# Performance work log

Hardware: AMD Instinct MI355X
Metric: run time of the kernel (lower is better)

The kernel has to match this reference:

```python
import jax, jax.numpy as jnp
import numpy as np

NUM_HEADS = 16
DIM_HIDDEN = 1024
DIM_ATTN = DIM_HIDDEN // NUM_HEADS  # 64
SCALE = DIM_ATTN ** (-0.5)
TOP_K = 32


def setup_inputs() -> dict:
    rng = jax.random.key(0)
    k1, k2, k3, k4, k5 = jax.random.split(rng, 5)
    b, sq, sk, d = 2, 2048, 2048, DIM_HIDDEN
    lim = 1.0 / np.sqrt(d)  # nn.Linear default init range
    return {
        "query": jax.random.normal(k1, (b, sq, d), jnp.float32),
        "key": jax.random.normal(k2, (b, sk, d), jnp.float32),
        "value": jax.random.normal(k3, (b, sk, d), jnp.float32),
        "Wq": jax.random.uniform(k4, (d, d), jnp.float32, -lim, lim),
        "Wk": jax.random.uniform(k5, (d, d), jnp.float32, -lim, lim),
    }


def _split_heads(x, b, s):
    # (b, s, D) -> (b, H, s, d_head)
    return x.reshape(b, s, NUM_HEADS, DIM_ATTN).transpose(0, 2, 1, 3)


def reference(query, key, value, Wq, Wk):
    b, sq, d = query.shape
    sk = key.shape[1]
    # nn.Linear: y = x @ W^T  (bias=False); V and out are Identity
    q = _split_heads(query @ Wq.T, b, sq)
    k = _split_heads(key @ Wk.T, b, sk)
    v = _split_heads(value, b, sk)
    # dense scores (b, H, sq, sk)
    scores = jnp.einsum('bhqa,bhka->bhqk', q, k) * SCALE
    # top-k sparsified softmax: keep entries >= k-th largest score per row
    top_vals = jax.lax.top_k(scores, TOP_K)[0]
    cutoff = top_vals[..., -1:]  # (b, H, sq, 1)
    masked = jnp.where(scores >= cutoff, scores, -jnp.inf)
    w = jax.nn.softmax(masked, axis=-1)
    e = jnp.einsum('bhqk,bhka->bhqa', w, v)
    return e.transpose(0, 2, 1, 3).reshape(b, sq, d)
```

## Files before the change

kernel.cpp:

```cpp
#include <hip/hip_runtime.h>
#include <cstdint>
#include <cstddef>

#define BB 2
#define HH 16
#define SS 2048
#define DD 1024
#define DA 64
#define TOPK 32
#define ROWS 4

__global__ __launch_bounds__(256, 4) void proj_kernel(const float* __restrict__ X0,
                                                      const float* __restrict__ W0,
                                                      float* __restrict__ O0,
                                                      const float* __restrict__ X1,
                                                      const float* __restrict__ W1,
                                                      float* __restrict__ O1) {
  const float* __restrict__ X = blockIdx.z ? X1 : X0;
  const float* __restrict__ W = blockIdx.z ? W1 : W0;
  float* __restrict__ O       = blockIdx.z ? O1 : O0;

  __shared__ float Ast[16][65];
  __shared__ float Bst[16][65];
  const int tid = threadIdx.x;
  const int tx = tid & 15, ty = tid >> 4;
  const int m0 = blockIdx.y * 64, n0 = blockIdx.x * 64;

  float res[4][4], acc[4][4];
#pragma unroll
  for (int i = 0; i < 4; ++i)
#pragma unroll
    for (int j = 0; j < 4; ++j) { res[i][j] = 0.f; acc[i][j] = 0.f; }

  const int srow = tid >> 2, skg = tid & 3;
  for (int k0 = 0; k0 < 1024; k0 += 16) {
    if (k0 == 384 || k0 == 768) {
#pragma unroll
      for (int i = 0; i < 4; ++i)
#pragma unroll
        for (int j = 0; j < 4; ++j) { res[i][j] = __fadd_rn(res[i][j], acc[i][j]); acc[i][j] = 0.f; }
    }
    {
      const float4 va = *(const float4*)(X + (size_t)(m0 + srow) * 1024 + k0 + skg * 4);
      Ast[skg * 4 + 0][srow] = va.x; Ast[skg * 4 + 1][srow] = va.y;
      Ast[skg * 4 + 2][srow] = va.z; Ast[skg * 4 + 3][srow] = va.w;
      const float4 vb = *(const float4*)(W + (size_t)(n0 + srow) * 1024 + k0 + skg * 4);
      Bst[skg * 4 + 0][srow] = vb.x; Bst[skg * 4 + 1][srow] = vb.y;
      Bst[skg * 4 + 2][srow] = vb.z; Bst[skg * 4 + 3][srow] = vb.w;
    }
    __syncthreads();
#pragma unroll
    for (int k = 0; k < 16; ++k) {
      float av[4], bv[4];
#pragma unroll
      for (int i = 0; i < 4; ++i) av[i] = Ast[k][ty * 4 + i];
#pragma unroll
      for (int j = 0; j < 4; ++j) bv[j] = Bst[k][tx * 4 + j];
#pragma unroll
      for (int i = 0; i < 4; ++i)
#pragma unroll
        for (int j = 0; j < 4; ++j) acc[i][j] = fmaf(av[i], bv[j], acc[i][j]);
    }
    __syncthreads();
  }

#pragma unroll
  for (int i = 0; i < 4; ++i) {
    const int m = m0 + ty * 4 + i;
    const int b = m >> 11, s = m & 2047;
#pragma unroll
    for (int j = 0; j < 4; ++j) {
      const int n = n0 + tx * 4 + j;
      const int h = n >> 6, da = n & 63;
      const float v = __fadd_rn(res[i][j], acc[i][j]);
      if (blockIdx.z) {
        O[(((size_t)((b * 16 + h) * 16 + (da >> 2)) * 2048 + s) << 2) + (da & 3)] = v;
      } else {
        O[(((size_t)(b * 16 + h) * 2048 + s) * 64 + da)] = v;
      }
    }
  }
}

__global__ __launch_bounds__(256) void attn_kernel(const float* __restrict__ Qp,
                                                   const float* __restrict__ Kp,
                                                   const float* __restrict__ V,
                                                   float* __restrict__ out) {
  __shared__ float Srow[ROWS * 2048];

  const int tid = threadIdx.x;
  const int w = tid >> 6, l = tid & 63;
  const int nwg = BB * HH * (SS / ROWS);
  const int bidx = (int)blockIdx.x;
  const int swz = (bidx & 7) * (nwg >> 3) + (bidx >> 3);
  const int bh = swz >> 9;
  const int rb = swz & 511;
  const int b = bh >> 4, h = bh & 15;
  const int r0 = rb * ROWS;

  const float* Ktb = Kp + (size_t)bh * (16 * 2048 * 4);

#pragma unroll 1
  for (int c = 0; c < 8; ++c) {
    const int key = tid + c * 256;

    float acc[ROWS][4];
#pragma unroll
    for (int r = 0; r < ROWS; ++r)
#pragma unroll
      for (int j = 0; j < 4; ++j) acc[r][j] = 0.f;

#pragma unroll
    for (int g = 0; g < 4; ++g) {
      float4 kt[4];
#pragma unroll
      for (int i = 0; i < 4; ++i)
        kt[i] = *(const float4*)(Ktb + (((size_t)(g * 4 + i) * 2048 + key) << 2));
#pragma unroll
      for (int r = 0; r < ROWS; ++r) {
        const float4* qp4 = (const float4*)(Qp + ((size_t)bh * SS + r0 + r) * DA);
        float4 q4[4];
#pragma unroll
        for (int i = 0; i < 4; ++i) q4[i] = qp4[g * 4 + i];
#pragma unroll
        for (int blk = 3; blk >= 0; --blk) {
          acc[r][0] = __fadd_rn(acc[r][0], __fmul_rn(q4[blk].x, kt[blk].x));
          acc[r][1] = __fadd_rn(acc[r][1], __fmul_rn(q4[blk].y, kt[blk].y));
          acc[r][2] = __fadd_rn(acc[r][2], __fmul_rn(q4[blk].z, kt[blk].z));
          acc[r][3] = __fadd_rn(acc[r][3], __fmul_rn(q4[blk].w, kt[blk].w));
        }
      }
    }
#pragma unroll
    for (int r = 0; r < ROWS; ++r) {
      const float s = __fadd_rn(__fadd_rn(acc[r][0], acc[r][1]),
                                __fadd_rn(acc[r][2], acc[r][3]));
      Srow[r * 2048 + key] = s * 0.125f;
    }
  }
  __syncthreads();

  const float* Vh = V + (size_t)b * SS * DD + h * DA;
  float* outh = out + ((size_t)(b * SS + r0 + w)) * DD + h * DA;

  {
    const int r = w;
    float sv[32];
#pragma unroll
    for (int i = 0; i < 32; ++i) sv[i] = Srow[r * 2048 + 64 * i + l];
    float* wl = &Srow[r * 2048];
    float* kl = &Srow[r * 2048 + 64];

    float mx = sv[0], mn = sv[0];
#pragma unroll
    for (int i = 1; i < 32; ++i) { mx = fmaxf(mx, sv[i]); mn = fminf(mn, sv[i]); }
#pragma unroll
    for (int off = 32; off >= 1; off >>= 1) {
      mx = fmaxf(mx, __shfl_xor(mx, off));
      mn = fminf(mn, __shfl_xor(mn, off));
    }

    float lo = mn, hi = mx + 1.0f;
    float cutoff = mn;
    for (int it = 0; ; ++it) {
      const float mid = 0.5f * (lo + hi);
      if (it >= 64 || !(mid > lo && mid < hi)) { cutoff = lo; break; }
      int c = 0;
#pragma unroll
      for (int i = 0; i < 32; ++i)
        c += (int)__popcll(__ballot(sv[i] >= mid));
      if (c == TOPK) {
        float cm = 3.0e38f;
#pragma unroll
        for (int i = 0; i < 32; ++i) if (sv[i] >= mid) cm = fminf(cm, sv[i]);
#pragma unroll
        for (int off = 32; off >= 1; off >>= 1) cm = fminf(cm, __shfl_xor(cm, off));
        cutoff = cm;
        break;
      }
      if (c > TOPK) lo = mid; else hi = mid;
    }

    float wv[32];
    float dpart = 0.f;
    int ckept = 0;
#pragma unroll
    for (int i = 0; i < 32; ++i) {
      const bool keep = (sv[i] >= cutoff);
      ckept += (int)__popcll(__ballot(keep));
      const float e = keep ? __expf(sv[i] - mx) : 0.f;
      wv[i] = e;
      dpart += e;
    }
    float denom = dpart;
#pragma unroll
    for (int off = 32; off >= 1; off >>= 1) denom += __shfl_xor(denom, off);
    const float inv_denom = 1.0f / denom;

    float e = 0.f;
    if (ckept <= 64) {
      int base = 0;
#pragma unroll
      for (int i = 0; i < 32; ++i) {
        const unsigned long long mball = __ballot(wv[i] > 0.f);
        if (wv[i] > 0.f) {
          const int pos = base + (int)__popcll(mball & ((1ull << l) - 1ull));
          wl[pos] = wv[i];
          kl[pos] = __int_as_float(64 * i + l);
        }
        base += (int)__popcll(mball);
      }
      asm volatile("s_waitcnt lgkmcnt(0)" ::: "memory");
      int i = 0;
      for (; i + 8 <= ckept; i += 8) {
        float ww[8]; int kk[8];
#pragma unroll
        for (int u = 0; u < 8; ++u) { ww[u] = wl[i + u]; kk[u] = __float_as_int(kl[i + u]); }
        float vv[8];
#pragma unroll
        for (int u = 0; u < 8; ++u) vv[u] = Vh[(size_t)kk[u] * DD + l];
#pragma unroll
        for (int u = 0; u < 8; ++u) e = fmaf(ww[u], vv[u], e);
      }
      for (; i < ckept; ++i) {
        const float ww = wl[i];
        const int kk = __float_as_int(kl[i]);
        e = fmaf(ww, Vh[(size_t)kk * DD + l], e);
      }
    } else {
#pragma unroll
      for (int i = 0; i < 32; ++i) Srow[r * 2048 + 64 * i + l] = wv[i];
      asm volatile("s_waitcnt lgkmcnt(0)" ::: "memory");
      for (int k = 0; k < 2048; ++k) {
        const float ww = Srow[r * 2048 + k];
        if (ww > 0.f) e = fmaf(ww, Vh[(size_t)k * DD + l], e);
      }
    }
    outh[l] = e * inv_denom;
  }
}

extern "C" void kernel_launch(void* const* d_in, const int* in_sizes, int n_in,
                              void* d_out, int out_size, void* d_ws, size_t ws_size,
                              hipStream_t stream) {
  const float* query = (const float*)d_in[0];
  const float* key   = (const float*)d_in[1];
  const float* value = (const float*)d_in[2];
  const float* Wq    = (const float*)d_in[3];
  const float* Wk    = (const float*)d_in[4];
  float* out = (float*)d_out;

  float* Qp = (float*)d_ws;
  float* Kp = Qp + (size_t)BB * HH * SS * DA;

  proj_kernel<<<dim3(16, 64, 2), 256, 0, stream>>>(query, Wq, Qp, key, Wk, Kp);
  attn_kernel<<<dim3(BB * HH * (SS / ROWS)), 256, 0, stream>>>(Qp, Kp, value, out);
}
```

Measured before the change: 944.7 us.

## Double-buffer shared-memory tiles in projection GEMM

Splits the projection kernel's shared tiles into two buffers. While the current tile is being multiplied, the next K-slice is loaded and stored into the other buffer, which cuts one barrier per iteration and overlaps global loads with FMAs. The row padding of 65 is dropped to 64, which may cause LDS bank conflicts on the transposed stores. The stage-ahead code is written as a macro inside a loop that is no longer unrolled.

Measured after the change: 877.6 us (median of 2 runs). 1.08x faster.

```diff
diff --git a/kernel.cpp b/kernel.cpp
--- a/kernel.cpp
+++ b/kernel.cpp
@@ -20,8 +20,8 @@
   const float* __restrict__ W = blockIdx.z ? W1 : W0;
   float* __restrict__ O       = blockIdx.z ? O1 : O0;
 
-  __shared__ float Ast[16][65];
-  __shared__ float Bst[16][65];
+  __shared__ float Ast[2][16][64];
+  __shared__ float Bst[2][16][64];
   const int tid = threadIdx.x;
   const int tx = tid & 15, ty = tid >> 4;
   const int m0 = blockIdx.y * 64, n0 = blockIdx.x * 64;
@@ -33,29 +33,38 @@
     for (int j = 0; j < 4; ++j) { res[i][j] = 0.f; acc[i][j] = 0.f; }
 
   const int srow = tid >> 2, skg = tid & 3;
-  for (int k0 = 0; k0 < 1024; k0 += 16) {
+
+#define STAGE(buf, kk)                                                        \
+  {                                                                           \
+    const float4 va = *(const float4*)(X + (size_t)(m0 + srow) * 1024 + (kk) + skg * 4); \
+    Ast[buf][skg * 4 + 0][srow] = va.x; Ast[buf][skg * 4 + 1][srow] = va.y;   \
+    Ast[buf][skg * 4 + 2][srow] = va.z; Ast[buf][skg * 4 + 3][srow] = va.w;   \
+    const float4 vb = *(const float4*)(W + (size_t)(n0 + srow) * 1024 + (kk) + skg * 4); \
+    Bst[buf][skg * 4 + 0][srow] = vb.x; Bst[buf][skg * 4 + 1][srow] = vb.y;   \
+    Bst[buf][skg * 4 + 2][srow] = vb.z; Bst[buf][skg * 4 + 3][srow] = vb.w;   \
+  }
+
+  STAGE(0, 0);
+  __syncthreads();
+
+#pragma unroll 1
+  for (int t = 0; t < 64; ++t) {
+    const int k0 = t * 16;
     if (k0 == 384 || k0 == 768) {
 #pragma unroll
       for (int i = 0; i < 4; ++i)
 #pragma unroll
         for (int j = 0; j < 4; ++j) { res[i][j] = __fadd_rn(res[i][j], acc[i][j]); acc[i][j] = 0.f; }
     }
-    {
-      const float4 va = *(const float4*)(X + (size_t)(m0 + srow) * 1024 + k0 + skg * 4);
-      Ast[skg * 4 + 0][srow] = va.x; Ast[skg * 4 + 1][srow] = va.y;
-      Ast[skg * 4 + 2][srow] = va.z; Ast[skg * 4 + 3][srow] = va.w;
-      const float4 vb = *(const float4*)(W + (size_t)(n0 + srow) * 1024 + k0 + skg * 4);
-      Bst[skg * 4 + 0][srow] = vb.x; Bst[skg * 4 + 1][srow] = vb.y;
-      Bst[skg * 4 + 2][srow] = vb.z; Bst[skg * 4 + 3][srow] = vb.w;
-    }
-    __syncthreads();
+    const int cur = t & 1;
+    if (t + 1 < 64) STAGE(cur ^ 1, k0 + 16);
 #pragma unroll
     for (int k = 0; k < 16; ++k) {
       float av[4], bv[4];
 #pragma unroll
-      for (int i = 0; i < 4; ++i) av[i] = Ast[k][ty * 4 + i];
-#pragma unroll
-      for (int j = 0; j < 4; ++j) bv[j] = Bst[k][tx * 4 + j];
+      for (int i = 0; i < 4; ++i) av[i] = Ast[cur][k][ty * 4 + i];
+#pragma unroll
+      for (int j = 0; j < 4; ++j) bv[j] = Bst[cur][k][tx * 4 + j];
 #pragma unroll
       for (int i = 0; i < 4; ++i)
 #pragma unroll
@@ -63,6 +72,7 @@
     }
     __syncthreads();
   }
+#undef STAGE
 
 #pragma unroll
   for (int i = 0; i < 4; ++i) {
```
